# Kernel optimization log

Hardware: AMD Instinct MI355X
Metric: run time of the kernel (lower is better)

Reference implementation:

```python
import jax, jax.numpy as jnp
import numpy as np

N = 50000
E = 800000
IN_CH = 128
HIDDEN = 32
HEADS = 4
OUT_CH = 64
NEG_SLOPE = 0.2


def setup_inputs() -> dict:
    key = jax.random.key(0)
    ks = jax.random.split(key, 12)
    x = jax.random.normal(ks[0], (N, IN_CH), dtype=jnp.float32)
    edge_index = jax.random.randint(ks[1], (2, E), 0, N, dtype=jnp.int64)
    # layer 1: GATConv(IN_CH, HIDDEN, heads=4, concat=True)
    s1 = 1.0 / np.sqrt(IN_CH)
    W1 = jax.random.normal(ks[2], (IN_CH, HEADS * HIDDEN), dtype=jnp.float32) * s1
    att_src1 = jax.random.normal(ks[3], (HEADS, HIDDEN), dtype=jnp.float32) * 0.1
    att_dst1 = jax.random.normal(ks[4], (HEADS, HIDDEN), dtype=jnp.float32) * 0.1
    b1 = jnp.zeros((HEADS * HIDDEN,), dtype=jnp.float32)
    # layer 2: GATConv(HEADS*HIDDEN, OUT_CH, heads=1, concat=False)
    s2 = 1.0 / np.sqrt(HEADS * HIDDEN)
    W2 = jax.random.normal(ks[5], (HEADS * HIDDEN, OUT_CH), dtype=jnp.float32) * s2
    att_src2 = jax.random.normal(ks[6], (1, OUT_CH), dtype=jnp.float32) * 0.1
    att_dst2 = jax.random.normal(ks[7], (1, OUT_CH), dtype=jnp.float32) * 0.1
    b2 = jnp.zeros((OUT_CH,), dtype=jnp.float32)
    return {"x": x, "edge_index": edge_index, "W1": W1, "att_src1": att_src1,
            "att_dst1": att_dst1, "b1": b1, "W2": W2, "att_src2": att_src2,
            "att_dst2": att_dst2, "b2": b2}


def gat_conv(x, src, dst, W, a_src, a_dst, bias, heads, out_ch, concat):
    n = x.shape[0]
    h = (x @ W).reshape(n, heads, out_ch)               # [N, H, C]
    alpha_s = jnp.sum(h * a_src[None], axis=-1)          # [N, H]
    alpha_d = jnp.sum(h * a_dst[None], axis=-1)          # [N, H]
    e = alpha_s[src] + alpha_d[dst]                      # [E, H]
    e = jnp.where(e > 0, e, NEG_SLOPE * e)               # leaky_relu(0.2)
    # segment softmax over incoming edges of each dst node
    e_max = jax.ops.segment_max(e, dst, num_segments=n)
    e_max = jnp.where(jnp.isfinite(e_max), e_max, 0.0)
    ex = jnp.exp(e - e_max[dst])
    denom = jax.ops.segment_sum(ex, dst, num_segments=n)
    alpha = ex / (denom[dst] + 1e-16)                    # [E, H]
    msg = h[src] * alpha[:, :, None]                     # [E, H, C]
    out = jax.ops.segment_sum(msg, dst, num_segments=n)  # [N, H, C]
    if concat:
        out = out.reshape(n, heads * out_ch)
    else:
        out = out.mean(axis=1)
    return out + bias


def reference(x, edge_index, W1, att_src1, att_dst1, b1, W2, att_src2, att_dst2, b2):
    n = x.shape[0]
    loop = jnp.arange(n, dtype=edge_index.dtype)
    src = jnp.concatenate([edge_index[0], loop])  # add self-loops (PyG default)
    dst = jnp.concatenate([edge_index[1], loop])
    h = gat_conv(x, src, dst, W1, att_src1, att_dst1, b1, HEADS, HIDDEN, True)
    h = jax.nn.elu(h)
    return gat_conv(h, src, dst, W2, att_src2, att_dst2, b2, 1, OUT_CH, False)
```

## Files before the change

### kernel.cpp

```cpp
#include <hip/hip_runtime.h>

#define NN    50000
#define NE    800000
#define NET   850000
#define NBUCK ((NN + 255) / 256)
#define MAXB  8192

typedef __fp16 half2_t __attribute__((ext_vector_type(2)));
typedef _Float16 half8 __attribute__((ext_vector_type(8)));
typedef float floatx4 __attribute__((ext_vector_type(4)));

__device__ __forceinline__ float lrelu(float v) { return fmaxf(v, 0.2f * v); }
__device__ __forceinline__ unsigned pk16(float a, float b) {
    half2_t h = __builtin_amdgcn_cvt_pkrtz(a, b);
    return __builtin_bit_cast(unsigned, h);
}
__device__ __forceinline__ float2 unpk16(unsigned u) {
    half2_t h = __builtin_bit_cast(half2_t, u);
    return make_float2((float)h.x, (float)h.y);
}

__global__ __launch_bounds__(256) void gemm1_mfma_kernel(
    const float* __restrict__ x, const _Float16* __restrict__ w1t,
    const float* __restrict__ att_s, const float* __restrict__ att_d,
    _Float16* __restrict__ h1h, float* __restrict__ as, float* __restrict__ ad)
{
    __shared__ _Float16 hs[64 * 128];
    const int t    = threadIdx.x;
    const int lane = t & 63;
    const int m    = lane & 15;
    const int q    = lane >> 4;
    const int wv   = t >> 6;
    const int gr0  = blockIdx.x * 64;
    const int rbase = gr0 + wv * 16;

    const int rme = rbase + m;
    const int rc  = rme < NN ? rme : NN - 1;
    const float* ap = x + (size_t)rc * 128 + q * 8;

    floatx4 acc[8];
#pragma unroll
    for (int nt = 0; nt < 8; nt++) acc[nt] = (floatx4){0.f, 0.f, 0.f, 0.f};

#pragma unroll
    for (int ks = 0; ks < 4; ks++) {
        const float4 f0 = *(const float4*)(ap + ks * 32);
        const float4 f1 = *(const float4*)(ap + ks * 32 + 4);
        const uint4 au = make_uint4(pk16(f0.x, f0.y), pk16(f0.z, f0.w),
                                    pk16(f1.x, f1.y), pk16(f1.z, f1.w));
        const half8 a = __builtin_bit_cast(half8, au);
#pragma unroll
        for (int nt = 0; nt < 8; nt++) {
            const half8 b = *(const half8*)(w1t + (nt * 16 + m) * 128 + ks * 32 + q * 8);
            acc[nt] = __builtin_amdgcn_mfma_f32_16x16x32_f16(a, b, acc[nt], 0, 0, 0);
        }
    }

    const int lrow0 = wv * 16 + q * 4;
#pragma unroll
    for (int nt = 0; nt < 8; nt++)
#pragma unroll
        for (int r = 0; r < 4; r++)
            hs[(lrow0 + r) * 128 + nt * 16 + m] = (_Float16)acc[nt][r];
    __syncthreads();

#pragma unroll
    for (int i = t; i < 1024; i += 256) {
        const int row = i >> 4;
        if (gr0 + row < NN)
            ((half8*)h1h)[(size_t)(gr0 + row) * 16 + (i & 15)] = ((const half8*)hs)[i];
    }

    const int arow = t >> 2, hd = t & 3;
    const int grow = gr0 + arow;
    float ps = 0.f, pd = 0.f;
    const half8*  hp8 = (const half8*)(hs + arow * 128 + hd * 32);
    const float4* s4  = (const float4*)(att_s + hd * 32);
    const float4* d4  = (const float4*)(att_d + hd * 32);
#pragma unroll
    for (int cc = 0; cc < 4; cc++) {
        const half8 hv = hp8[cc];
        const float4 a = s4[cc * 2], b = s4[cc * 2 + 1];
        const float4 c = d4[cc * 2], e = d4[cc * 2 + 1];
        ps += (float)hv[0]*a.x + (float)hv[1]*a.y + (float)hv[2]*a.z + (float)hv[3]*a.w
            + (float)hv[4]*b.x + (float)hv[5]*b.y + (float)hv[6]*b.z + (float)hv[7]*b.w;
        pd += (float)hv[0]*c.x + (float)hv[1]*c.y + (float)hv[2]*c.z + (float)hv[3]*c.w
            + (float)hv[4]*e.x + (float)hv[5]*e.y + (float)hv[6]*e.z + (float)hv[7]*e.w;
    }
    if (grow < NN) {
        as[grow * 4 + hd] = ps;
        ad[grow * 4 + hd] = pd;
    }
}

__global__ __launch_bounds__(256) void gemm2_mfma_kernel(
    const _Float16* __restrict__ ah, const _Float16* __restrict__ w2t,
    const float* __restrict__ att_s, const float* __restrict__ att_d,
    _Float16* __restrict__ h2h, float* __restrict__ as, float* __restrict__ ad)
{
    __shared__ _Float16 hs[64 * 64];
    const int t    = threadIdx.x;
    const int lane = t & 63;
    const int m    = lane & 15;
    const int q    = lane >> 4;
    const int wv   = t >> 6;
    const int gr0  = blockIdx.x * 64;
    const int rbase = gr0 + wv * 16;

    const int rme = rbase + m;
    const int rc  = rme < NN ? rme : NN - 1;
    const _Float16* ap = ah + (size_t)rc * 128 + q * 8;

    floatx4 acc[4];
#pragma unroll
    for (int nt = 0; nt < 4; nt++) acc[nt] = (floatx4){0.f, 0.f, 0.f, 0.f};

#pragma unroll
    for (int ks = 0; ks < 4; ks++) {
        const half8 a = *(const half8*)(ap + ks * 32);
#pragma unroll
        for (int nt = 0; nt < 4; nt++) {
            const half8 b = *(const half8*)(w2t + (nt * 16 + m) * 128 + ks * 32 + q * 8);
            acc[nt] = __builtin_amdgcn_mfma_f32_16x16x32_f16(a, b, acc[nt], 0, 0, 0);
        }
    }

    const int lrow0 = wv * 16 + q * 4;
#pragma unroll
    for (int nt = 0; nt < 4; nt++)
#pragma unroll
        for (int r = 0; r < 4; r++)
            hs[(lrow0 + r) * 64 + nt * 16 + m] = (_Float16)acc[nt][r];
    __syncthreads();

#pragma unroll
    for (int i = t; i < 512; i += 256) {
        const int row = i >> 3;
        if (gr0 + row < NN)
            ((half8*)h2h)[(size_t)(gr0 + row) * 8 + (i & 7)] = ((const half8*)hs)[i];
    }

    const int arow = t >> 2, sg = t & 3;
    const int grow = gr0 + arow;
    float ps = 0.f, pd = 0.f;
    const half8*  hp8 = (const half8*)(hs + arow * 64 + sg * 16);
    const float4* s4  = (const float4*)(att_s + sg * 16);
    const float4* d4  = (const float4*)(att_d + sg * 16);
#pragma unroll
    for (int cc = 0; cc < 2; cc++) {
        const half8 hv = hp8[cc];
        const float4 a = s4[cc * 2], b = s4[cc * 2 + 1];
        const float4 c = d4[cc * 2], e = d4[cc * 2 + 1];
        ps += (float)hv[0]*a.x + (float)hv[1]*a.y + (float)hv[2]*a.z + (float)hv[3]*a.w
            + (float)hv[4]*b.x + (float)hv[5]*b.y + (float)hv[6]*b.z + (float)hv[7]*b.w;
        pd += (float)hv[0]*c.x + (float)hv[1]*c.y + (float)hv[2]*c.z + (float)hv[3]*c.w
            + (float)hv[4]*e.x + (float)hv[5]*e.y + (float)hv[6]*e.z + (float)hv[7]*e.w;
    }
    ps += __shfl_down(ps, 2);  pd += __shfl_down(pd, 2);
    ps += __shfl_down(ps, 1);  pd += __shfl_down(pd, 1);
    if (sg == 0 && grow < NN) { as[grow] = ps; ad[grow] = pd; }
}

__global__ __launch_bounds__(1024) void bin_kernel(const int* __restrict__ ei,
                                                   const float* __restrict__ W1,
                                                   const float* __restrict__ W2,
                                                   _Float16* __restrict__ w1t,
                                                   _Float16* __restrict__ w2t,
                                                   int* __restrict__ bcnt,
                                                   unsigned* __restrict__ pairs)
{
    if (blockIdx.x < 24) {
        const int idx = blockIdx.x * 1024 + threadIdx.x;
        if (idx < 16384) {
            const int k = idx >> 7, n = idx & 127;
            w1t[n * 128 + k] = (_Float16)W1[idx];
        } else {
            const int j = idx - 16384;
            const int k = j >> 6, n = j & 63;
            w2t[n * 128 + k] = (_Float16)W2[j];
        }
    }

    __shared__ int hist[NBUCK], base[NBUCK], cur[NBUCK];
    const int t = threadIdx.x;
    if (t < NBUCK) { hist[t] = 0; cur[t] = 0; }
    __syncthreads();
    const int e = blockIdx.x * 1024 + t;
    int s = 0, d = 0, bk = 0;
    const bool ok = e < NET;
    if (ok) {
        if (e < NE) { s = ei[e]; d = ei[NE + e]; } else { s = d = e - NE; }
        bk = d >> 8;
        atomicAdd(&hist[bk], 1);
    }
    __syncthreads();
    if (t < NBUCK && hist[t]) base[t] = atomicAdd(&bcnt[t], hist[t]);
    __syncthreads();
    if (ok) {
        const int r = atomicAdd(&cur[bk], 1);
        pairs[(size_t)bk * MAXB + base[bk] + r] =
            (unsigned)s | ((unsigned)(d & 255) << 16);
    }
}

__global__ __launch_bounds__(1024) void bsort_kernel(
    const int* __restrict__ bcnt, const unsigned* __restrict__ pairs,
    int* __restrict__ row_beg, int* __restrict__ row_end,
    int* __restrict__ col)
{
    __shared__ int hist[256], cur[256], sh[256];
    __shared__ int outl[MAXB];
    const int b = blockIdx.x, t = threadIdx.x;
    const int m = bcnt[b];
    const int gbase = b * MAXB;
    if (t < 256) hist[t] = 0;
    __syncthreads();
    for (int i = t; i < m; i += 1024)
        atomicAdd(&hist[pairs[gbase + i] >> 16], 1);
    __syncthreads();
    if (t < 256) sh[t] = hist[t];
    __syncthreads();
#pragma unroll
    for (int off = 1; off < 256; off <<= 1) {
        int u = (t < 256 && t >= off) ? sh[t - off] : 0;
        __syncthreads();
        if (t < 256) sh[t] += u;
        __syncthreads();
    }
    if (t < 256) {
        const int ex = sh[t] - hist[t];
        cur[t] = ex;
        const int node = (b << 8) + t;
        if (node < NN) {
            row_beg[node] = gbase + ex;
            row_end[node] = gbase + ex + hist[t];
        }
    }
    __syncthreads();
    for (int i = t; i < m; i += 1024) {
        const unsigned p = pairs[gbase + i];
        const int r = atomicAdd(&cur[p >> 16], 1);
        outl[r] = (int)(p & 0xFFFFu);
    }
    __syncthreads();
    for (int i = t; i < m; i += 1024) col[gbase + i] = outl[i];
}

__global__ __launch_bounds__(256) void agg1_fused_kernel(
    const int* __restrict__ row_beg, const int* __restrict__ row_end,
    const int* __restrict__ col, const unsigned* __restrict__ hh,
    const float* __restrict__ as1, const float* __restrict__ ad1,
    const float* __restrict__ b1, unsigned* __restrict__ acth)
{
    __shared__ float wbuf[4][64 * 4];
    const int wv   = threadIdx.x >> 6;
    const int d    = __builtin_amdgcn_readfirstlane((blockIdx.x * 256 + threadIdx.x) >> 6);
    const int lane = threadIdx.x & 63;
    const int head = lane >> 4;
    const int beg = row_beg[d], end = row_end[d];
    const float4 ad4 = ((const float4*)ad1)[d];
    float* wb = wbuf[wv];

    float acc0 = 0.f, acc1 = 0.f, den = 0.f;

    for (int jb = beg; jb < end; jb += 64) {
        const int cnt = min(64, end - jb);
        {
            const int sl = col[jb + min(lane, cnt - 1)];
            const float4 a = ((const float4*)as1)[sl];
            float4 w4;
            w4.x = __expf(lrelu(a.x + ad4.x));
            w4.y = __expf(lrelu(a.y + ad4.y));
            w4.z = __expf(lrelu(a.z + ad4.z));
            w4.w = __expf(lrelu(a.w + ad4.w));
            ((float4*)wb)[lane] = w4;
        }
        __asm__ volatile("s_waitcnt lgkmcnt(0)" ::: "memory");

        int k = 0;
        for (; k + 16 <= cnt; k += 16) {
            float    w[16];
            unsigned g[16];
#pragma unroll
            for (int u = 0; u < 16; u++) {
                const int s = col[jb + k + u];
                w[u] = wb[(k + u) * 4 + head];
                g[u] = hh[s * 64 + lane];
            }
#pragma unroll
            for (int u = 0; u < 16; u++) {
                const float2 g2 = unpk16(g[u]);
                den  += w[u];
                acc0 += w[u] * g2.x;
                acc1 += w[u] * g2.y;
            }
        }
        for (; k + 4 <= cnt; k += 4) {
            float    w[4];
            unsigned g[4];
#pragma unroll
            for (int u = 0; u < 4; u++) {
                const int s = col[jb + k + u];
                w[u] = wb[(k + u) * 4 + head];
                g[u] = hh[s * 64 + lane];
            }
#pragma unroll
            for (int u = 0; u < 4; u++) {
                const float2 g2 = unpk16(g[u]);
                den  += w[u];
                acc0 += w[u] * g2.x;
                acc1 += w[u] * g2.y;
            }
        }
        for (; k < cnt; k++) {
            const float w = wb[k * 4 + head];
            const float2 g2 = unpk16(hh[col[jb + k] * 64 + lane]);
            den  += w;
            acc0 += w * g2.x;
            acc1 += w * g2.y;
        }
        __asm__ volatile("" ::: "memory");
    }
    const float2 bb  = ((const float2*)b1)[lane];
    const float  inv = 1.f / (den + 1e-16f);
    float v0 = acc0 * inv + bb.x;
    float v1 = acc1 * inv + bb.y;
    v0 = v0 > 0.f ? v0 : (__expf(v0) - 1.f);
    v1 = v1 > 0.f ? v1 : (__expf(v1) - 1.f);
    acth[d * 64 + lane] = pk16(v0, v1);
}

__global__ __launch_bounds__(256) void agg2_fused_kernel(
    const int* __restrict__ row_beg, const int* __restrict__ row_end,
    const int* __restrict__ col, const _Float16* __restrict__ h,
    const float* __restrict__ as2, const float* __restrict__ ad2,
    const float* __restrict__ b2, float* __restrict__ out)
{
    __shared__ float wbuf[4][64];
    const int wv   = threadIdx.x >> 6;
    const int d    = __builtin_amdgcn_readfirstlane((blockIdx.x * 256 + threadIdx.x) >> 6);
    const int lane = threadIdx.x & 63;
    const int beg = row_beg[d], end = row_end[d];
    const float add = ad2[d];
    float* wb = wbuf[wv];

    float acc = 0.f, den = 0.f;

    for (int jb = beg; jb < end; jb += 64) {
        const int cnt = min(64, end - jb);
        {
            const int sl = col[jb + min(lane, cnt - 1)];
            wb[lane] = __expf(lrelu(as2[sl] + add));
        }
        __asm__ volatile("s_waitcnt lgkmcnt(0)" ::: "memory");

        int k = 0;
        for (; k + 16 <= cnt; k += 16) {
            float w[16], g[16];
#pragma unroll
            for (int u = 0; u < 16; u++) {
                const int s = col[jb + k + u];
                w[u] = wb[k + u];
                g[u] = (float)h[s * 64 + lane];
            }
#pragma unroll
            for (int u = 0; u < 16; u++) {
                den += w[u];
                acc += w[u] * g[u];
            }
        }
        for (; k + 4 <= cnt; k += 4) {
            float w[4], g[4];
#pragma unroll
            for (int u = 0; u < 4; u++) {
                const int s = col[jb + k + u];
                w[u] = wb[k + u];
                g[u] = (float)h[s * 64 + lane];
            }
#pragma unroll
            for (int u = 0; u < 4; u++) {
                den += w[u];
                acc += w[u] * g[u];
            }
        }
        for (; k < cnt; k++) {
            const float w = wb[k];
            den += w;
            acc += w * (float)h[col[jb + k] * 64 + lane];
        }
        __asm__ volatile("" ::: "memory");
    }
    out[d * 64 + lane] = acc / (den + 1e-16f) + b2[lane];
}

extern "C" void kernel_launch(void* const* d_in, const int* in_sizes, int n_in,
                              void* d_out, int out_size, void* d_ws, size_t ws_size,
                              hipStream_t stream)
{
    const float* x    = (const float*)d_in[0];
    const int*   ei   = (const int*)  d_in[1];
    const float* W1   = (const float*)d_in[2];
    const float* at_s1= (const float*)d_in[3];
    const float* at_d1= (const float*)d_in[4];
    const float* b1   = (const float*)d_in[5];
    const float* W2   = (const float*)d_in[6];
    const float* at_s2= (const float*)d_in[7];
    const float* at_d2= (const float*)d_in[8];
    const float* b2   = (const float*)d_in[9];
    float*       out  = (float*)d_out;

    const size_t NPAD = (size_t)NBUCK * MAXB;

    float* fw   = (float*)d_ws;
    float* as1  = fw;
    float* ad1  = as1  + NN * 4;
    float* as2  = ad1  + NN * 4;
    float* ad2  = as2  + NN;
    _Float16* h1h   = (_Float16*)(ad2 + NN);
    _Float16* act1h = h1h  + (size_t)NN * 128;
    _Float16* h2h   = act1h+ (size_t)NN * 128;
    _Float16* w1t   = h2h  + (size_t)NN * 64;
    _Float16* w2t   = w1t  + 16384;
    int*   row_beg = (int*)(w2t + 8192);
    int*   row_end = row_beg + NN;
    int*   col     = row_end + NN;
    int*   bcnt    = col + NPAD;
    unsigned* pairs = (unsigned*)(bcnt + 256);

    hipMemsetAsync(bcnt, 0, 256 * sizeof(int), stream);

    const int eg1024 = (NET + 1023) / 1024;
    const int gemm_grid = (NN + 63) / 64;
    const int node_wave_grid = NN / 4;

    bin_kernel  <<<eg1024, 1024, 0, stream>>>(ei, W1, W2, w1t, w2t, bcnt, pairs);
    bsort_kernel<<<NBUCK, 1024, 0, stream>>>(bcnt, pairs, row_beg, row_end, col);

    gemm1_mfma_kernel<<<gemm_grid, 256, 0, stream>>>(x, w1t, at_s1, at_d1, h1h, as1, ad1);
    agg1_fused_kernel<<<node_wave_grid, 256, 0, stream>>>(row_beg, row_end, col,
                        (const unsigned*)h1h, as1, ad1, b1, (unsigned*)act1h);

    gemm2_mfma_kernel<<<gemm_grid, 256, 0, stream>>>(act1h, w2t, at_s2, at_d2, h2h, as2, ad2);
    agg2_fused_kernel<<<node_wave_grid, 256, 0, stream>>>(row_beg, row_end, col,
                        h2h, as2, ad2, b2, out);
}
```

Before: 212.1 us.

## Merge edge binning and weight transpose into the first GEMM launch

Fuses the edge-binning kernel and the weight conversion into the layer-1 GEMM kernel by assigning extra blocks to binning, using 256-thread blocks. Each GEMM block now transposes the full W1 into w1t before its MFMA loop, with a block barrier in between, so the GEMM and binning run concurrently in one launch instead of two serialized ones. The cost is redundant W1 conversion work in every GEMM block. There is also a race: a block only synchronizes on its own writes to w1t, while other blocks may be writing the same global values at the same time.

```diff
diff --git a/kernel.cpp b/kernel.cpp
--- a/kernel.cpp
+++ b/kernel.cpp
@@ -5,6 +5,8 @@
 #define NET   850000
 #define NBUCK ((NN + 255) / 256)
 #define MAXB  8192
+#define GB    ((NN + 63) / 64)
+#define BINB  ((NET + 255) / 256)
 
 typedef __fp16 half2_t __attribute__((ext_vector_type(2)));
 typedef _Float16 half8 __attribute__((ext_vector_type(8)));
@@ -20,13 +22,49 @@
     return make_float2((float)h.x, (float)h.y);
 }
 
-__global__ __launch_bounds__(256) void gemm1_mfma_kernel(
-    const float* __restrict__ x, const _Float16* __restrict__ w1t,
+__global__ __launch_bounds__(256) void gemm1_bin_kernel(
+    const float* __restrict__ x, const float* __restrict__ W1,
+    const float* __restrict__ W2, const int* __restrict__ ei,
     const float* __restrict__ att_s, const float* __restrict__ att_d,
-    _Float16* __restrict__ h1h, float* __restrict__ as, float* __restrict__ ad)
-{
+    _Float16* __restrict__ w1t, _Float16* __restrict__ w2t,
+    _Float16* __restrict__ h1h, float* __restrict__ as, float* __restrict__ ad,
+    int* __restrict__ bcnt, unsigned* __restrict__ pairs)
+{
+    const int t = threadIdx.x;
+
+    if (blockIdx.x >= GB) {
+        const int bb = blockIdx.x - GB;
+        if (bb < 32) {
+            const int idx = bb * 256 + t;
+            const int k = idx >> 6, n = idx & 63;
+            w2t[n * 128 + k] = (_Float16)W2[idx];
+        }
+        __shared__ int hist[NBUCK], base[NBUCK], cur[NBUCK];
+        if (t < NBUCK) { hist[t] = 0; cur[t] = 0; }
+        __syncthreads();
+        const int e = bb * 256 + t;
+        int s = 0, d = 0, bk = 0;
+        const bool ok = e < NET;
+        if (ok) {
+            if (e < NE) { s = ei[e]; d = ei[NE + e]; } else { s = d = e - NE; }
+            bk = d >> 8;
+            atomicAdd(&hist[bk], 1);
+        }
+        __syncthreads();
+        if (t < NBUCK && hist[t]) base[t] = atomicAdd(&bcnt[t], hist[t]);
+        __syncthreads();
+        if (ok) {
+            const int r = atomicAdd(&cur[bk], 1);
+            pairs[(size_t)bk * MAXB + base[bk] + r] =
+                (unsigned)s | ((unsigned)(d & 255) << 16);
+        }
+        return;
+    }
+
+    for (int idx = t; idx < 16384; idx += 256)
+        w1t[(idx & 127) * 128 + (idx >> 7)] = (_Float16)W1[idx];
+
     __shared__ _Float16 hs[64 * 128];
-    const int t    = threadIdx.x;
     const int lane = t & 63;
     const int m    = lane & 15;
     const int q    = lane >> 4;
@@ -41,6 +79,8 @@
     floatx4 acc[8];
 #pragma unroll
     for (int nt = 0; nt < 8; nt++) acc[nt] = (floatx4){0.f, 0.f, 0.f, 0.f};
+
+    __syncthreads();
 
 #pragma unroll
     for (int ks = 0; ks < 4; ks++) {
@@ -159,48 +199,6 @@
     ps += __shfl_down(ps, 2);  pd += __shfl_down(pd, 2);
     ps += __shfl_down(ps, 1);  pd += __shfl_down(pd, 1);
     if (sg == 0 && grow < NN) { as[grow] = ps; ad[grow] = pd; }
-}
-
-__global__ __launch_bounds__(1024) void bin_kernel(const int* __restrict__ ei,
-                                                   const float* __restrict__ W1,
-                                                   const float* __restrict__ W2,
-                                                   _Float16* __restrict__ w1t,
-                                                   _Float16* __restrict__ w2t,
-                                                   int* __restrict__ bcnt,
-                                                   unsigned* __restrict__ pairs)
-{
-    if (blockIdx.x < 24) {
-        const int idx = blockIdx.x * 1024 + threadIdx.x;
-        if (idx < 16384) {
-            const int k = idx >> 7, n = idx & 127;
-            w1t[n * 128 + k] = (_Float16)W1[idx];
-        } else {
-            const int j = idx - 16384;
-            const int k = j >> 6, n = j & 63;
-            w2t[n * 128 + k] = (_Float16)W2[j];
-        }
-    }
-
-    __shared__ int hist[NBUCK], base[NBUCK], cur[NBUCK];
-    const int t = threadIdx.x;
-    if (t < NBUCK) { hist[t] = 0; cur[t] = 0; }
-    __syncthreads();
-    const int e = blockIdx.x * 1024 + t;
-    int s = 0, d = 0, bk = 0;
-    const bool ok = e < NET;
-    if (ok) {
-        if (e < NE) { s = ei[e]; d = ei[NE + e]; } else { s = d = e - NE; }
-        bk = d >> 8;
-        atomicAdd(&hist[bk], 1);
-    }
-    __syncthreads();
-    if (t < NBUCK && hist[t]) base[t] = atomicAdd(&bcnt[t], hist[t]);
-    __syncthreads();
-    if (ok) {
-        const int r = atomicAdd(&cur[bk], 1);
-        pairs[(size_t)bk * MAXB + base[bk] + r] =
-            (unsigned)s | ((unsigned)(d & 255) << 16);
-    }
 }
 
 __global__ __launch_bounds__(1024) void bsort_kernel(
@@ -429,18 +427,15 @@
 
     hipMemsetAsync(bcnt, 0, 256 * sizeof(int), stream);
 
-    const int eg1024 = (NET + 1023) / 1024;
-    const int gemm_grid = (NN + 63) / 64;
     const int node_wave_grid = NN / 4;
 
-    bin_kernel  <<<eg1024, 1024, 0, stream>>>(ei, W1, W2, w1t, w2t, bcnt, pairs);
-    bsort_kernel<<<NBUCK, 1024, 0, stream>>>(bcnt, pairs, row_beg, row_end, col);
-
-    gemm1_mfma_kernel<<<gemm_grid, 256, 0, stream>>>(x, w1t, at_s1, at_d1, h1h, as1, ad1);
+    gemm1_bin_kernel<<<GB + BINB, 256, 0, stream>>>(x, W1, W2, ei, at_s1, at_d1,
+                        w1t, w2t, h1h, as1, ad1, bcnt, pairs);
+    bsort_kernel    <<<NBUCK, 1024, 0, stream>>>(bcnt, pairs, row_beg, row_end, col);
     agg1_fused_kernel<<<node_wave_grid, 256, 0, stream>>>(row_beg, row_end, col,
                         (const unsigned*)h1h, as1, ad1, b1, (unsigned*)act1h);
 
-    gemm2_mfma_kernel<<<gemm_grid, 256, 0, stream>>>(act1h, w2t, at_s2, at_d2, h2h, as2, ad2);
+    gemm2_mfma_kernel<<<GB, 256, 0, stream>>>(act1h, w2t, at_s2, at_d2, h2h, as2, ad2);
     agg2_fused_kernel<<<node_wave_grid, 256, 0, stream>>>(row_beg, row_end, col,
                         h2h, as2, ad2, b2, out);
 }
```

Result: slower. 298.4 us (+40.7%).

## Slice feature tables by channel chunk and use 16-bit column indices in aggregation

Applied to the files above, without the earlier changes.

The GEMM kernels now write projected features into per-slice planes, 32 fp16 channels per plane for layer 1 and 16 for layer 2. Each aggregation block handles one slice for four destination nodes, with lane groups working on different edges and combined by cross-lane shuffles. Column indices are stored as 16-bit values, and the grid is four times larger, so each slice's gather touches a smaller, more cache-friendly table. The cost is redundant weight exp computation per slice, more blocks, and extra shuffle reductions.

```diff
diff --git a/kernel.cpp b/kernel.cpp
--- a/kernel.cpp
+++ b/kernel.cpp
@@ -23,7 +23,7 @@
 __global__ __launch_bounds__(256) void gemm1_mfma_kernel(
     const float* __restrict__ x, const _Float16* __restrict__ w1t,
     const float* __restrict__ att_s, const float* __restrict__ att_d,
-    _Float16* __restrict__ h1h, float* __restrict__ as, float* __restrict__ ad)
+    unsigned* __restrict__ hsl, float* __restrict__ as, float* __restrict__ ad)
 {
     __shared__ _Float16 hs[64 * 128];
     const int t    = threadIdx.x;
@@ -66,9 +66,10 @@
 
 #pragma unroll
     for (int i = t; i < 1024; i += 256) {
-        const int row = i >> 4;
+        const int row = i >> 4, u = i & 15;
         if (gr0 + row < NN)
-            ((half8*)h1h)[(size_t)(gr0 + row) * 16 + (i & 15)] = ((const half8*)hs)[i];
+            ((half8*)hsl)[(size_t)(u >> 2) * (NN * 4) + (size_t)(gr0 + row) * 4 + (u & 3)]
+                = ((const half8*)hs)[i];
     }
 
     const int arow = t >> 2, hd = t & 3;
@@ -96,7 +97,7 @@
 __global__ __launch_bounds__(256) void gemm2_mfma_kernel(
     const _Float16* __restrict__ ah, const _Float16* __restrict__ w2t,
     const float* __restrict__ att_s, const float* __restrict__ att_d,
-    _Float16* __restrict__ h2h, float* __restrict__ as, float* __restrict__ ad)
+    unsigned* __restrict__ h2sl, float* __restrict__ as, float* __restrict__ ad)
 {
     __shared__ _Float16 hs[64 * 64];
     const int t    = threadIdx.x;
@@ -135,9 +136,10 @@
 
 #pragma unroll
     for (int i = t; i < 512; i += 256) {
-        const int row = i >> 3;
+        const int row = i >> 3, u = i & 7;
         if (gr0 + row < NN)
-            ((half8*)h2h)[(size_t)(gr0 + row) * 8 + (i & 7)] = ((const half8*)hs)[i];
+            ((half8*)h2sl)[(size_t)(u >> 1) * (NN * 2) + (size_t)(gr0 + row) * 2 + (u & 1)]
+                = ((const half8*)hs)[i];
     }
 
     const int arow = t >> 2, sg = t & 3;
@@ -206,7 +208,7 @@
 __global__ __launch_bounds__(1024) void bsort_kernel(
     const int* __restrict__ bcnt, const unsigned* __restrict__ pairs,
     int* __restrict__ row_beg, int* __restrict__ row_end,
-    int* __restrict__ col)
+    unsigned short* __restrict__ col16)
 {
     __shared__ int hist[256], cur[256], sh[256];
     __shared__ int outl[MAXB];
@@ -243,22 +245,25 @@
         outl[r] = (int)(p & 0xFFFFu);
     }
     __syncthreads();
-    for (int i = t; i < m; i += 1024) col[gbase + i] = outl[i];
+    for (int i = t; i < m; i += 1024) col16[gbase + i] = (unsigned short)outl[i];
 }
 
 __global__ __launch_bounds__(256) void agg1_fused_kernel(
     const int* __restrict__ row_beg, const int* __restrict__ row_end,
-    const int* __restrict__ col, const unsigned* __restrict__ hh,
+    const unsigned short* __restrict__ col16, const unsigned* __restrict__ hsl,
     const float* __restrict__ as1, const float* __restrict__ ad1,
     const float* __restrict__ b1, unsigned* __restrict__ acth)
 {
-    __shared__ float wbuf[4][64 * 4];
-    const int wv   = threadIdx.x >> 6;
-    const int d    = __builtin_amdgcn_readfirstlane((blockIdx.x * 256 + threadIdx.x) >> 6);
-    const int lane = threadIdx.x & 63;
-    const int head = lane >> 4;
+    __shared__ float wbuf[4][64];
+    const int wv    = threadIdx.x >> 6;
+    const int lane  = threadIdx.x & 63;
+    const int slice = blockIdx.x & 3;
+    const int d     = __builtin_amdgcn_readfirstlane((blockIdx.x >> 2) * 4 + wv);
+    const int grp   = lane >> 4;
+    const int dw    = lane & 15;
     const int beg = row_beg[d], end = row_end[d];
-    const float4 ad4 = ((const float4*)ad1)[d];
+    const float adh = ad1[d * 4 + slice];
+    const unsigned* hp = hsl + (size_t)slice * (NN * 16);
     float* wb = wbuf[wv];
 
     float acc0 = 0.f, acc1 = 0.f, den = 0.f;
@@ -266,131 +271,105 @@
     for (int jb = beg; jb < end; jb += 64) {
         const int cnt = min(64, end - jb);
         {
-            const int sl = col[jb + min(lane, cnt - 1)];
-            const float4 a = ((const float4*)as1)[sl];
-            float4 w4;
-            w4.x = __expf(lrelu(a.x + ad4.x));
-            w4.y = __expf(lrelu(a.y + ad4.y));
-            w4.z = __expf(lrelu(a.z + ad4.z));
-            w4.w = __expf(lrelu(a.w + ad4.w));
-            ((float4*)wb)[lane] = w4;
+            const int sl = col16[jb + min(lane, cnt - 1)];
+            wb[lane] = __expf(lrelu(as1[sl * 4 + slice] + adh));
         }
         __asm__ volatile("s_waitcnt lgkmcnt(0)" ::: "memory");
 
-        int k = 0;
-        for (; k + 16 <= cnt; k += 16) {
-            float    w[16];
-            unsigned g[16];
-#pragma unroll
-            for (int u = 0; u < 16; u++) {
-                const int s = col[jb + k + u];
-                w[u] = wb[(k + u) * 4 + head];
-                g[u] = hh[s * 64 + lane];
+        for (int k = 0; k < cnt; k += 32) {
+            float    w[8];
+            unsigned g[8];
+#pragma unroll
+            for (int u = 0; u < 8; u++) {
+                const int e  = k + u * 4 + grp;
+                const int ec = min(e, cnt - 1);
+                const int s  = col16[jb + ec];
+                w[u] = (e < cnt) ? wb[ec] : 0.f;
+                g[u] = hp[(size_t)s * 16 + dw];
             }
 #pragma unroll
-            for (int u = 0; u < 16; u++) {
+            for (int u = 0; u < 8; u++) {
                 const float2 g2 = unpk16(g[u]);
                 den  += w[u];
                 acc0 += w[u] * g2.x;
                 acc1 += w[u] * g2.y;
             }
         }
-        for (; k + 4 <= cnt; k += 4) {
-            float    w[4];
-            unsigned g[4];
-#pragma unroll
-            for (int u = 0; u < 4; u++) {
-                const int s = col[jb + k + u];
-                w[u] = wb[(k + u) * 4 + head];
-                g[u] = hh[s * 64 + lane];
+        __asm__ volatile("" ::: "memory");
+    }
+    den  += __shfl_xor(den, 16);  den  += __shfl_xor(den, 32);
+    acc0 += __shfl_xor(acc0, 16); acc0 += __shfl_xor(acc0, 32);
+    acc1 += __shfl_xor(acc1, 16); acc1 += __shfl_xor(acc1, 32);
+
+    const float2 bb  = ((const float2*)b1)[slice * 16 + dw];
+    const float  inv = 1.f / (den + 1e-16f);
+    float v0 = acc0 * inv + bb.x;
+    float v1 = acc1 * inv + bb.y;
+    v0 = v0 > 0.f ? v0 : (__expf(v0) - 1.f);
+    v1 = v1 > 0.f ? v1 : (__expf(v1) - 1.f);
+    if (grp == 0)
+        acth[(size_t)d * 64 + slice * 16 + dw] = pk16(v0, v1);
+}
+
+__global__ __launch_bounds__(256) void agg2_fused_kernel(
+    const int* __restrict__ row_beg, const int* __restrict__ row_end,
+    const unsigned short* __restrict__ col16, const unsigned* __restrict__ h2sl,
+    const float* __restrict__ as2, const float* __restrict__ ad2,
+    const float* __restrict__ b2, float* __restrict__ out)
+{
+    __shared__ float wbuf[4][64];
+    const int wv    = threadIdx.x >> 6;
+    const int lane  = threadIdx.x & 63;
+    const int slice = blockIdx.x & 3;
+    const int d     = __builtin_amdgcn_readfirstlane((blockIdx.x >> 2) * 4 + wv);
+    const int grp   = lane >> 3;
+    const int dw    = lane & 7;
+    const int beg = row_beg[d], end = row_end[d];
+    const float add = ad2[d];
+    const unsigned* hp = h2sl + (size_t)slice * (NN * 8);
+    float* wb = wbuf[wv];
+
+    float acc0 = 0.f, acc1 = 0.f, den = 0.f;
+
+    for (int jb = beg; jb < end; jb += 64) {
+        const int cnt = min(64, end - jb);
+        {
+            const int sl = col16[jb + min(lane, cnt - 1)];
+            wb[lane] = __expf(lrelu(as2[sl] + add));
+        }
+        __asm__ volatile("s_waitcnt lgkmcnt(0)" ::: "memory");
+
+        {
+            float    w[8];
+            unsigned g[8];
+#pragma unroll
+            for (int u = 0; u < 8; u++) {
+                const int e  = u * 8 + grp;
+                const int ec = min(e, cnt - 1);
+                const int s  = col16[jb + ec];
+                w[u] = (e < cnt) ? wb[ec] : 0.f;
+                g[u] = hp[(size_t)s * 8 + dw];
             }
 #pragma unroll
-            for (int u = 0; u < 4; u++) {
+            for (int u = 0; u < 8; u++) {
                 const float2 g2 = unpk16(g[u]);
                 den  += w[u];
                 acc0 += w[u] * g2.x;
                 acc1 += w[u] * g2.y;
             }
         }
-        for (; k < cnt; k++) {
-            const float w = wb[k * 4 + head];
-            const float2 g2 = unpk16(hh[col[jb + k] * 64 + lane]);
-            den  += w;
-            acc0 += w * g2.x;
-            acc1 += w * g2.y;
-        }
         __asm__ volatile("" ::: "memory");
     }
-    const float2 bb  = ((const float2*)b1)[lane];
-    const float  inv = 1.f / (den + 1e-16f);
-    float v0 = acc0 * inv + bb.x;
-    float v1 = acc1 * inv + bb.y;
-    v0 = v0 > 0.f ? v0 : (__expf(v0) - 1.f);
-    v1 = v1 > 0.f ? v1 : (__expf(v1) - 1.f);
-    acth[d * 64 + lane] = pk16(v0, v1);
-}
-
-__global__ __launch_bounds__(256) void agg2_fused_kernel(
-    const int* __restrict__ row_beg, const int* __restrict__ row_end,
-    const int* __restrict__ col, const _Float16* __restrict__ h,
-    const float* __restrict__ as2, const float* __restrict__ ad2,
-    const float* __restrict__ b2, float* __restrict__ out)
-{
-    __shared__ float wbuf[4][64];
-    const int wv   = threadIdx.x >> 6;
-    const int d    = __builtin_amdgcn_readfirstlane((blockIdx.x * 256 + threadIdx.x) >> 6);
-    const int lane = threadIdx.x & 63;
-    const int beg = row_beg[d], end = row_end[d];
-    const float add = ad2[d];
-    float* wb = wbuf[wv];
-
-    float acc = 0.f, den = 0.f;
-
-    for (int jb = beg; jb < end; jb += 64) {
-        const int cnt = min(64, end - jb);
-        {
-            const int sl = col[jb + min(lane, cnt - 1)];
-            wb[lane] = __expf(lrelu(as2[sl] + add));
-        }
-        __asm__ volatile("s_waitcnt lgkmcnt(0)" ::: "memory");
-
-        int k = 0;
-        for (; k + 16 <= cnt; k += 16) {
-            float w[16], g[16];
-#pragma unroll
-            for (int u = 0; u < 16; u++) {
-                const int s = col[jb + k + u];
-                w[u] = wb[k + u];
-                g[u] = (float)h[s * 64 + lane];
-            }
-#pragma unroll
-            for (int u = 0; u < 16; u++) {
-                den += w[u];
-                acc += w[u] * g[u];
-            }
-        }
-        for (; k + 4 <= cnt; k += 4) {
-            float w[4], g[4];
-#pragma unroll
-            for (int u = 0; u < 4; u++) {
-                const int s = col[jb + k + u];
-                w[u] = wb[k + u];
-                g[u] = (float)h[s * 64 + lane];
-            }
-#pragma unroll
-            for (int u = 0; u < 4; u++) {
-                den += w[u];
-                acc += w[u] * g[u];
-            }
-        }
-        for (; k < cnt; k++) {
-            const float w = wb[k];
-            den += w;
-            acc += w * (float)h[col[jb + k] * 64 + lane];
-        }
-        __asm__ volatile("" ::: "memory");
-    }
-    out[d * 64 + lane] = acc / (den + 1e-16f) + b2[lane];
+    den  += __shfl_xor(den, 8);  den  += __shfl_xor(den, 16);  den  += __shfl_xor(den, 32);
+    acc0 += __shfl_xor(acc0, 8); acc0 += __shfl_xor(acc0, 16); acc0 += __shfl_xor(acc0, 32);
+    acc1 += __shfl_xor(acc1, 8); acc1 += __shfl_xor(acc1, 16); acc1 += __shfl_xor(acc1, 32);
+
+    if (grp == 0) {
+        const float2 bb  = ((const float2*)b2)[slice * 8 + dw];
+        const float  inv = 1.f / (den + 1e-16f);
+        ((float2*)out)[(size_t)d * 32 + slice * 8 + dw] =
+            make_float2(acc0 * inv + bb.x, acc1 * inv + bb.y);
+    }
 }
 
 extern "C" void kernel_launch(void* const* d_in, const int* in_sizes, int n_in,
@@ -416,31 +395,31 @@
     float* ad1  = as1  + NN * 4;
     float* as2  = ad1  + NN * 4;
     float* ad2  = as2  + NN;
-    _Float16* h1h   = (_Float16*)(ad2 + NN);
-    _Float16* act1h = h1h  + (size_t)NN * 128;
-    _Float16* h2h   = act1h+ (size_t)NN * 128;
-    _Float16* w1t   = h2h  + (size_t)NN * 64;
-    _Float16* w2t   = w1t  + 16384;
+    unsigned* hsl  = (unsigned*)(ad2 + NN);
+    _Float16* act1h = (_Float16*)(hsl + (size_t)NN * 64);
+    unsigned* h2sl = (unsigned*)(act1h + (size_t)NN * 128);
+    _Float16* w1t  = (_Float16*)(h2sl + (size_t)NN * 32);
+    _Float16* w2t  = w1t + 16384;
     int*   row_beg = (int*)(w2t + 8192);
     int*   row_end = row_beg + NN;
-    int*   col     = row_end + NN;
-    int*   bcnt    = col + NPAD;
+    unsigned short* col16 = (unsigned short*)(row_end + NN);
+    int*   bcnt    = (int*)(col16 + NPAD);
     unsigned* pairs = (unsigned*)(bcnt + 256);
 
     hipMemsetAsync(bcnt, 0, 256 * sizeof(int), stream);
 
     const int eg1024 = (NET + 1023) / 1024;
     const int gemm_grid = (NN + 63) / 64;
-    const int node_wave_grid = NN / 4;
+    const int agg_grid  = (NN / 4) * 4;
 
     bin_kernel  <<<eg1024, 1024, 0, stream>>>(ei, W1, W2, w1t, w2t, bcnt, pairs);
-    bsort_kernel<<<NBUCK, 1024, 0, stream>>>(bcnt, pairs, row_beg, row_end, col);
-
-    gemm1_mfma_kernel<<<gemm_grid, 256, 0, stream>>>(x, w1t, at_s1, at_d1, h1h, as1, ad1);
-    agg1_fused_kernel<<<node_wave_grid, 256, 0, stream>>>(row_beg, row_end, col,
-                        (const unsigned*)h1h, as1, ad1, b1, (unsigned*)act1h);
-
-    gemm2_mfma_kernel<<<gemm_grid, 256, 0, stream>>>(act1h, w2t, at_s2, at_d2, h2h, as2, ad2);
-    agg2_fused_kernel<<<node_wave_grid, 256, 0, stream>>>(row_beg, row_end, col,
-                        h2h, as2, ad2, b2, out);
-}
+    bsort_kernel<<<NBUCK, 1024, 0, stream>>>(bcnt, pairs, row_beg, row_end, col16);
+
+    gemm1_mfma_kernel<<<gemm_grid, 256, 0, stream>>>(x, w1t, at_s1, at_d1, hsl, as1, ad1);
+    agg1_fused_kernel<<<agg_grid, 256, 0, stream>>>(row_beg, row_end, col16, hsl,
+                        as1, ad1, b1, (unsigned*)act1h);
+
+    gemm2_mfma_kernel<<<gemm_grid, 256, 0, stream>>>(act1h, w2t, at_s2, at_d2, h2sl, as2, ad2);
+    agg2_fused_kernel<<<agg_grid, 256, 0, stream>>>(row_beg, row_end, col16, h2sl,
+                        as2, ad2, b2, out);
+}
```

New measurement: 338.4 us. 59.6% more time.
